# Kernel optimization log

Measured on AMD Instinct MI355X. Metric: run time of the kernel, lower is better.

The kernel has to match this reference:

```python
import jax, jax.numpy as jnp
import numpy as np

N, E, D = 50000, 800000, 128

def setup_inputs() -> dict:
    key = jax.random.key(0)
    ks = jax.random.split(key, 8)
    s = 0.02
    x = jax.random.normal(ks[0], (N, D), dtype=jnp.float32)
    edge_index = jax.random.randint(ks[1], (2, E), 0, N, dtype=jnp.int64)
    Wn = jax.random.normal(ks[2], (D, D), dtype=jnp.float32) * s
    bn = jax.random.normal(ks[3], (D,), dtype=jnp.float32) * s
    We = jax.random.normal(ks[4], (D, 2 * D), dtype=jnp.float32) * s
    be = jax.random.normal(ks[5], (D,), dtype=jnp.float32) * s
    Wu = jax.random.normal(ks[6], (D, 3 * D), dtype=jnp.float32) * s
    bu = jax.random.normal(ks[7], (D,), dtype=jnp.float32) * s
    return {"x": x, "edge_index": edge_index, "Wn": Wn, "bn": bn,
            "We": We, "be": be, "Wu": Wu, "bu": bu}

def reference(x, edge_index, Wn, bn, We, be, Wu, bu):
    n = x.shape[0]
    # 1. per-node linear transform (torch Linear: x @ W.T + b)
    node = x @ Wn.T + bn                                   # [N, D]
    src, dst = edge_index[0], edge_index[1]
    # 2. per-edge embedding from concatenated endpoint node embeddings
    edge_in = jnp.concatenate([node[src], node[dst]], axis=1)  # [E, 2D]
    edge_emb = edge_in @ We.T + be                          # [E, D]
    # 3. scatter-sum neighbor node embeddings and incident edge embeddings to src vertex
    nbr_sum = jax.ops.segment_sum(node[dst], src, num_segments=n)    # [N, D]
    edge_sum = jax.ops.segment_sum(edge_emb, src, num_segments=n)   # [N, D]
    pre_gelu = jnp.concatenate([node, nbr_sum, edge_sum], axis=1)    # [N, 3D]
    # 4-5. GELU (exact, matching torch nn.GELU default) + final linear
    out = jax.nn.gelu(pre_gelu, approximate=False) @ Wu.T + bu       # [N, D]
    return out
```

## Files before the change

kernel.cpp:

```cpp
#include <hip/hip_runtime.h>
#include <hip/hip_bf16.h>
#include <math.h>

typedef __attribute__((ext_vector_type(8))) short short8;
typedef __attribute__((ext_vector_type(4))) float f32x4;

#define CAP8 16
#define EPT  8

__device__ __forceinline__ float bf2f(unsigned short u) {
    union { unsigned int i; float f; } c; c.i = ((unsigned int)u) << 16; return c.f;
}
__device__ __forceinline__ unsigned short f2bf(float f) {
    __hip_bfloat16 h = __float2bfloat16(f);
    union { __hip_bfloat16 h; unsigned short u; } c; c.h = h; return c.u;
}
__device__ __forceinline__ float gelu_exact(float x) {
    return 0.5f * x * (1.0f + erff(x * 0.7071067811865475f));
}
__device__ __forceinline__ short8 ldcvt8(const float* p) {
    float4 f0 = *(const float4*)p;
    float4 f1 = *(const float4*)(p + 4);
    short8 a;
    a[0] = (short)f2bf(f0.x); a[1] = (short)f2bf(f0.y);
    a[2] = (short)f2bf(f0.z); a[3] = (short)f2bf(f0.w);
    a[4] = (short)f2bf(f1.x); a[5] = (short)f2bf(f1.y);
    a[6] = (short)f2bf(f1.z); a[7] = (short)f2bf(f1.w);
    return a;
}
__device__ __forceinline__ int swz(int row, int colbyte) {
    return row * 256 + (colbyte ^ ((row & 7) << 4));
}

__device__ __forceinline__ int detect_flag(const int* ei, int E) {
    int orv = 0;
    int lim = (E < 64) ? E : 64;
    for (int i = 0; i < lim; i++) orv |= ei[2 * i + 1];
    return (orv == 0) ? 1 : 0;
}
__device__ __forceinline__ int ld_src(const int* ei, int flag, int E, int e) {
    if (flag) { int2 p = *(const int2*)(ei + 2 * (size_t)e); return p.x; }
    return ei[e];
}
__device__ __forceinline__ int ld_dst(const int* ei, int flag, int E, int e) {
    if (flag) { int2 p = *(const int2*)(ei + 2 * (size_t)(E + e)); return p.x; }
    return ei[E + e];
}

__launch_bounds__(256)
__global__ void init_kernel(const float* __restrict__ Wn, const float* __restrict__ We,
                            const float* __restrict__ Wu,
                            unsigned short* __restrict__ Wnb, unsigned short* __restrict__ Web,
                            unsigned short* __restrict__ Wub,
                            int* __restrict__ cursor8, int N) {
    const int stride = gridDim.x * 256;
    const int t = blockIdx.x * 256 + threadIdx.x;
    for (int i = t; i < 8 * N; i += stride) cursor8[i] = 0;
    for (int i = t; i < 128 * 128; i += stride) Wnb[i] = f2bf(Wn[i]);
    for (int i = t; i < 128 * 256; i += stride) Web[i] = f2bf(We[i]);
    for (int i = t; i < 128 * 384; i += stride) Wub[i] = f2bf(Wu[i]);
}

__device__ __forceinline__ void gemm1_body(int bid,
                                           const float* __restrict__ x,
                                           const unsigned short* __restrict__ Wnb,
                                           const float* __restrict__ bias,
                                           unsigned short* __restrict__ node,
                                           unsigned short* __restrict__ Apre0,
                                           int N) {
    const int v0 = bid * 64;
    const int wave = threadIdx.x >> 6;
    const int lane = threadIdx.x & 63;
    const int m    = lane & 15;
    const int kq   = lane >> 4;

    short8 B[2][4];
#pragma unroll
    for (int ntl = 0; ntl < 2; ntl++) {
        const int j = (wave * 2 + ntl) * 16 + m;
#pragma unroll
        for (int kb = 0; kb < 4; kb++)
            B[ntl][kb] = *(const short8*)(Wnb + (size_t)j * 128 + kb * 32 + kq * 8);
    }

    f32x4 acc[4][2];
#pragma unroll
    for (int mt = 0; mt < 4; mt++)
#pragma unroll
        for (int ntl = 0; ntl < 2; ntl++) acc[mt][ntl] = (f32x4){0.f,0.f,0.f,0.f};

#pragma unroll
    for (int kb = 0; kb < 4; kb++) {
#pragma unroll
        for (int mt = 0; mt < 4; mt++) {
            const int row = v0 + mt * 16 + m;
            short8 a = (short8){0,0,0,0,0,0,0,0};
            if (row < N) a = ldcvt8(x + (size_t)row * 128 + kb * 32 + kq * 8);
#pragma unroll
            for (int ntl = 0; ntl < 2; ntl++)
                acc[mt][ntl] = __builtin_amdgcn_mfma_f32_16x16x32_bf16(a, B[ntl][kb], acc[mt][ntl], 0, 0, 0);
        }
    }

    const int ocol = lane & 15;
#pragma unroll
    for (int mt = 0; mt < 4; mt++) {
#pragma unroll
        for (int ntl = 0; ntl < 2; ntl++) {
            const int col = (wave * 2 + ntl) * 16 + ocol;
            const float bval = bias[col];
#pragma unroll
            for (int r = 0; r < 4; r++) {
                const int row = v0 + mt * 16 + (lane >> 4) * 4 + r;
                if (row < N) {
                    const float v = acc[mt][ntl][r] + bval;
                    node[(size_t)row * 128 + col]  = f2bf(v);
                    Apre0[(size_t)row * 128 + col] = f2bf(gelu_exact(v));
                }
            }
        }
    }
}

__launch_bounds__(256)
__global__ void fused_a(const float* __restrict__ x,
                        const unsigned short* __restrict__ Wnb,
                        const float* __restrict__ bn,
                        unsigned short* __restrict__ node,
                        unsigned short* __restrict__ Apre0,
                        const int* __restrict__ ei,
                        int* __restrict__ cursor8,
                        unsigned short* __restrict__ csr8,
                        int E, int N, int mblocks) {
    const int grp = blockIdx.x >> 3;
    if ((grp % 3) != 0) {
        const int g1 = grp - grp / 3 - 1;
        const int mid = g1 * 8 + (int)(blockIdx.x & 7);
        if (mid < mblocks) gemm1_body(mid, x, Wnb, bn, node, Apre0, N);
        return;
    }
    __shared__ int sflag;
    if (threadIdx.x == 0) sflag = detect_flag(ei, E);
    __syncthreads();
    const int fgrp = grp / 3;
    const int b = (int)(blockIdx.x & 7);
    const int e0 = (fgrp * 8 + b) * (256 * EPT) + (int)threadIdx.x;

    int sv[EPT], dv[EPT], p[EPT];
    bool ok[EPT];
#pragma unroll
    for (int k = 0; k < EPT; k++) {
        const int e = e0 + k * 256;
        ok[k] = (e < E);
        sv[k] = 0; dv[k] = 0; p[k] = CAP8;
        if (ok[k]) { sv[k] = ld_src(ei, sflag, E, e); dv[k] = ld_dst(ei, sflag, E, e); }
    }
#pragma unroll
    for (int k = 0; k < EPT; k++) {
        ok[k] = ok[k] && (unsigned)sv[k] < (unsigned)N && (unsigned)dv[k] < (unsigned)N;
        if (ok[k]) p[k] = atomicAdd(&cursor8[(size_t)b * N + sv[k]], 1);
    }
#pragma unroll
    for (int k = 0; k < EPT; k++) {
        if (ok[k] && p[k] < CAP8)
            csr8[((size_t)b * N + sv[k]) * CAP8 + p[k]] = (unsigned short)dv[k];
    }
}

#define G_ISSUE(I, B) { \
    const int vl_ = wave * 8 + (I); \
    dg_[B] = (v0 + vl_ < N) ? degI[vl_] : 0; \
    _Pragma("unroll") \
    for (int u = 0; u < 8; u++) { \
        const int r_ = way + u * 4; \
        const int id_ = (r_ < dg_[B]) ? (int)listT[vl_ * 128 + r_] : 0; \
        A_[B][u] = *(const short8*)(node + (size_t)id_ * 128 + sl * 8); \
    } }

#define G_CONSUME(I, B) { \
    const int vl_ = wave * 8 + (I); \
    const int v_  = v0 + vl_; \
    const int deg_ = dg_[B]; \
    float acc_[8] = {0.f,0.f,0.f,0.f,0.f,0.f,0.f,0.f}; \
    _Pragma("unroll") \
    for (int u = 0; u < 8; u++) { \
        const int r_ = way + u * 4; \
        if (r_ < deg_) { \
            _Pragma("unroll") \
            for (int k = 0; k < 8; k++) acc_[k] += bf2f((unsigned short)A_[B][u][k]); \
        } } \
    for (int base_ = 32; base_ < deg_; base_ += 32) {   \
        _Pragma("unroll") \
        for (int u = 0; u < 8; u++) { \
            const int r_ = base_ + way + u * 4; \
            const int id_ = (r_ < deg_) ? (int)listT[vl_ * 128 + r_] : 0; \
            short8 t_ = *(const short8*)(node + (size_t)id_ * 128 + sl * 8); \
            if (r_ < deg_) { \
                _Pragma("unroll") \
                for (int k = 0; k < 8; k++) acc_[k] += bf2f((unsigned short)t_[k]); \
            } } } \
    _Pragma("unroll") \
    for (int k = 0; k < 8; k++) { \
        acc_[k] += __shfl_xor(acc_[k], 16); \
        acc_[k] += __shfl_xor(acc_[k], 32); \
    } \
    if (v_ < N) { \
        if (way == 0) { \
            short8 o_; \
            _Pragma("unroll") \
            for (int k = 0; k < 8; k++) o_[k] = (short)f2bf(acc_[k]); \
            *(short8*)((char*)nbrT + swz(vl_, sl * 16)) = o_; \
        } else if (way == 1) { \
            short8 o_; \
            _Pragma("unroll") \
            for (int k = 0; k < 8; k++) o_[k] = (short)f2bf(gelu_exact(acc_[k])); \
            *(short8*)((char*)gnbrT + swz(vl_, sl * 16)) = o_; \
        } } }

__launch_bounds__(256)
__global__ void fused_b(const int* __restrict__ cursor8,
                        const unsigned short* __restrict__ csr8,
                        const unsigned short* __restrict__ node,
                        const unsigned short* __restrict__ Apre0,
                        const unsigned short* __restrict__ Web,
                        const float* __restrict__ be,
                        const unsigned short* __restrict__ Wub,
                        const float* __restrict__ bu,
                        float* __restrict__ out, int N) {
    __shared__ unsigned short nbrT [32 * 128];
    __shared__ unsigned short gnbrT[32 * 128];
    __shared__ unsigned short scratch[32 * 128];
    __shared__ int   degBv[32][8];
    __shared__ int   degI[32];
    __shared__ float degF[32];

    const int v0   = blockIdx.x * 32;
    const int tid  = threadIdx.x;
    const int wave = tid >> 6;
    const int lane = tid & 63;
    const int m    = lane & 15;
    const int kq   = lane >> 4;
    const bool full = (v0 + 32 <= N);

    {
        const int vi = tid >> 3, b = tid & 7;
        const int v = v0 + vi;
        int c = (v < N) ? cursor8[(size_t)b * N + v] : 0;
        degBv[vi][b] = (c > CAP8) ? CAP8 : c;
    }
    __syncthreads();
    if (tid < 32) {
        int s = 0;
#pragma unroll
        for (int b = 0; b < 8; b++) s += degBv[tid][b];
        degI[tid] = s; degF[tid] = (float)s;
    }
    __syncthreads();

    {
        unsigned short* listT = scratch;
#pragma unroll
        for (int i = 0; i < 8; i++) {
            const int vl = wave * 8 + i;
            const int v  = v0 + vl;
            if (v >= N) continue;
            const int slot0 = lane, slot1 = lane + 64;
            const unsigned short i0 = csr8[((size_t)(slot0 >> 4) * N + v) * CAP8 + (slot0 & 15)];
            const unsigned short i1 = csr8[((size_t)(slot1 >> 4) * N + v) * CAP8 + (slot1 & 15)];
            const bool vd0 = (slot0 & 15) < degBv[vl][slot0 >> 4];
            const bool vd1 = (slot1 & 15) < degBv[vl][slot1 >> 4];
            const unsigned long long m0 = __ballot(vd0);
            const unsigned long long m1 = __ballot(vd1);
            const unsigned long long below = (1ull << lane) - 1ull;
            const int n0 = __popcll(m0);
            if (vd0) listT[vl * 128 + __popcll(m0 & below)] = i0;
            if (vd1) listT[vl * 128 + n0 + __popcll(m1 & below)] = i1;
        }
        asm volatile("s_waitcnt lgkmcnt(0)" ::: "memory");

        const int way = lane >> 4, sl = lane & 15;
        short8 A_[2][8];
        int dg_[2];
        G_ISSUE(0, 0)
        G_ISSUE(1, 1)
        G_CONSUME(0, 0) G_ISSUE(2, 0)
        G_CONSUME(1, 1) G_ISSUE(3, 1)
        G_CONSUME(2, 0) G_ISSUE(4, 0)
        G_CONSUME(3, 1) G_ISSUE(5, 1)
        G_CONSUME(4, 0) G_ISSUE(6, 0)
        G_CONSUME(5, 1) G_ISSUE(7, 1)
        G_CONSUME(6, 0)
        G_CONSUME(7, 1)
    }
    __syncthreads();

    {
        f32x4 acc2[2][2];
#pragma unroll
        for (int mt = 0; mt < 2; mt++)
#pragma unroll
            for (int ntl = 0; ntl < 2; ntl++) acc2[mt][ntl] = (f32x4){0.f,0.f,0.f,0.f};

#pragma unroll
        for (int kb = 0; kb < 4; kb++) {
            short8 B0[2], B1[2], an[2], ab[2];
#pragma unroll
            for (int ntl = 0; ntl < 2; ntl++) {
                const int j = (wave * 2 + ntl) * 16 + m;
                B0[ntl] = *(const short8*)(Web + (size_t)j * 256 + kb * 32 + kq * 8);
                B1[ntl] = *(const short8*)(Web + (size_t)j * 256 + 128 + kb * 32 + kq * 8);
            }
#pragma unroll
            for (int mt = 0; mt < 2; mt++) {
                const int lrow = mt * 16 + m;
                const int row  = v0 + lrow;
                an[mt] = (full || row < N) ? *(const short8*)(node + (size_t)row * 128 + kb * 32 + kq * 8)
                                           : (short8){0,0,0,0,0,0,0,0};
                ab[mt] = *(const short8*)((const char*)nbrT + swz(lrow, kb * 64 + kq * 16));
            }
#pragma unroll
            for (int mt = 0; mt < 2; mt++) {
                const float dg = degF[mt * 16 + m];
#pragma unroll
                for (int k = 0; k < 8; k++)
                    an[mt][k] = (short)f2bf(dg * bf2f((unsigned short)an[mt][k]));
            }
#pragma unroll
            for (int mt = 0; mt < 2; mt++)
#pragma unroll
                for (int ntl = 0; ntl < 2; ntl++) {
                    acc2[mt][ntl] = __builtin_amdgcn_mfma_f32_16x16x32_bf16(an[mt], B0[ntl], acc2[mt][ntl], 0, 0, 0);
                    acc2[mt][ntl] = __builtin_amdgcn_mfma_f32_16x16x32_bf16(ab[mt], B1[ntl], acc2[mt][ntl], 0, 0, 0);
                }
        }

        const int ocol = lane & 15;
#pragma unroll
        for (int mt = 0; mt < 2; mt++) {
#pragma unroll
            for (int ntl = 0; ntl < 2; ntl++) {
                const int col = (wave * 2 + ntl) * 16 + ocol;
                const float bval = be[col];
#pragma unroll
                for (int r = 0; r < 4; r++) {
                    const int lrow = mt * 16 + (lane >> 4) * 4 + r;
                    const float dg = degF[lrow];
                    const float vv = gelu_exact(acc2[mt][ntl][r] + dg * bval);
                    *(unsigned short*)((char*)scratch + swz(lrow, col * 2)) = f2bf(vv);
                }
            }
        }
    }
    __syncthreads();

    {
        f32x4 acc3[2][2];
#pragma unroll
        for (int mt = 0; mt < 2; mt++)
#pragma unroll
            for (int ntl = 0; ntl < 2; ntl++) acc3[mt][ntl] = (f32x4){0.f,0.f,0.f,0.f};

#pragma unroll
        for (int s = 0; s < 3; s++) {
#pragma unroll
            for (int kb = 0; kb < 4; kb++) {
                short8 B3[2], a[2];
#pragma unroll
                for (int ntl = 0; ntl < 2; ntl++) {
                    const int j = (wave * 2 + ntl) * 16 + m;
                    B3[ntl] = *(const short8*)(Wub + (size_t)j * 384 + s * 128 + kb * 32 + kq * 8);
                }
#pragma unroll
                for (int mt = 0; mt < 2; mt++) {
                    const int lrow = mt * 16 + m;
                    const int row  = v0 + lrow;
                    if (s == 0) {
                        a[mt] = (full || row < N) ? *(const short8*)(Apre0 + (size_t)row * 128 + kb * 32 + kq * 8)
                                                  : (short8){0,0,0,0,0,0,0,0};
                    } else if (s == 1) {
                        a[mt] = *(const short8*)((const char*)gnbrT + swz(lrow, kb * 64 + kq * 16));
                    } else {
                        a[mt] = *(const short8*)((const char*)scratch + swz(lrow, kb * 64 + kq * 16));
                    }
                }
#pragma unroll
                for (int mt = 0; mt < 2; mt++)
#pragma unroll
                    for (int ntl = 0; ntl < 2; ntl++)
                        acc3[mt][ntl] = __builtin_amdgcn_mfma_f32_16x16x32_bf16(a[mt], B3[ntl], acc3[mt][ntl], 0, 0, 0);
            }
        }

        const int ocol = lane & 15;
#pragma unroll
        for (int mt = 0; mt < 2; mt++) {
#pragma unroll
            for (int ntl = 0; ntl < 2; ntl++) {
                const int col = (wave * 2 + ntl) * 16 + ocol;
                const float bval = bu[col];
#pragma unroll
                for (int r = 0; r < 4; r++) {
                    const int row = v0 + mt * 16 + (lane >> 4) * 4 + r;
                    if (row < N)
                        out[(size_t)row * 128 + col] = acc3[mt][ntl][r] + bval;
                }
            }
        }
    }
}

extern "C" void kernel_launch(void* const* d_in, const int* in_sizes, int n_in,
                              void* d_out, int out_size, void* d_ws, size_t ws_size,
                              hipStream_t stream) {
    const float* x  = (const float*)d_in[0];
    const int*   ei = (const int*)d_in[1];
    const float* Wn = (const float*)d_in[2];
    const float* bn = (const float*)d_in[3];
    const float* We = (const float*)d_in[4];
    const float* be = (const float*)d_in[5];
    const float* Wu = (const float*)d_in[6];
    const float* bu = (const float*)d_in[7];

    const int N = in_sizes[0] / 128;
    const int E = in_sizes[1] / 2;

    char* ws = (char*)d_ws;
    size_t off = 0;
    unsigned short* node  = (unsigned short*)(ws + off); off += (size_t)N * 128 * 2;
    unsigned short* Apre0 = (unsigned short*)(ws + off); off += (size_t)N * 128 * 2;
    off = (off + 255) & ~(size_t)255;
    int* cursor8 = (int*)(ws + off);                     off += (size_t)8 * N * 4;
    off = (off + 255) & ~(size_t)255;
    unsigned short* csr8 = (unsigned short*)(ws + off);  off += (size_t)8 * N * CAP8 * 2;
    off = (off + 255) & ~(size_t)255;
    unsigned short* Wnb = (unsigned short*)(ws + off);   off += (size_t)128 * 128 * 2;
    unsigned short* Web = (unsigned short*)(ws + off);   off += (size_t)128 * 256 * 2;
    unsigned short* Wub = (unsigned short*)(ws + off);   off += (size_t)128 * 384 * 2;

    const int mblocks = (N + 63) / 64;
    const int eblocks = (E + 256 * EPT - 1) / (256 * EPT);
    const int fgroups = (eblocks + 7) / 8;
    const int ggroups = (mblocks + 7) / 8;
    const int tgroups = fgroups + ggroups;
    const int grid_a  = tgroups * 8;

    init_kernel<<<512, 256, 0, stream>>>(Wn, We, Wu, Wnb, Web, Wub, cursor8, N);
    fused_a<<<grid_a, 256, 0, stream>>>(x, Wnb, bn, node, Apre0, ei, cursor8, csr8, E, N, mblocks);
    fused_b<<<(N + 31) / 32, 256, 0, stream>>>(cursor8, csr8, node, Apre0, Web, be, Wub, bu, (float*)d_out, N);
}
```

Baseline: 249.1 us.

## Stage neighbor gathers through LDS with async global_load_lds ring pipeline

Replaces the register double-buffered neighbor gather with direct global-to-LDS loads (global_load_lds) into a six-deep per-wave staging ring. Gathers are split into chunks of 8 neighbors and consumed after a vmcnt wait, with XOR swizzling on chunk columns to avoid bank conflicts. The goal is to keep more gather requests in flight without register pressure. The cost is 48KB of extra LDS, which may reduce occupancy, plus reliance on exact vmcnt accounting.

Measured after the change: 283.3 us. 13.7% more time.

```diff
diff --git a/kernel.cpp b/kernel.cpp
--- a/kernel.cpp
+++ b/kernel.cpp
@@ -30,6 +30,12 @@
 }
 __device__ __forceinline__ int swz(int row, int colbyte) {
     return row * 256 + (colbyte ^ ((row & 7) << 4));
+}
+
+typedef const __attribute__((address_space(1))) void* gas_p;
+typedef __attribute__((address_space(3))) void* las_p;
+__device__ __forceinline__ void gload_lds16(const void* g, void* l) {
+    __builtin_amdgcn_global_load_lds((gas_p)g, (las_p)l, 16, 0, 0);
 }
 
 __device__ __forceinline__ int detect_flag(const int* ei, int E) {
@@ -167,55 +173,67 @@
     }
 }
 
-#define G_ISSUE(I, B) { \
-    const int vl_ = wave * 8 + (I); \
-    dg_[B] = (v0 + vl_ < N) ? degI[vl_] : 0; \
+#define ISSUE(J) { \
+    constexpr int j_ = (J); \
+    if constexpr (j_ < 32) { \
+        const int vl_  = wv8 + (j_ >> 2); \
+        const int nb0_ = (j_ & 3) * 8; \
+        const int dgv_ = degI[vl_]; \
+        _Pragma("unroll") \
+        for (int i_ = 0; i_ < 2; i_++) { \
+            const int r_  = (lane >> 4) + 4 * i_;       \
+            const int n_  = nb0_ + r_; \
+            const int id_ = (n_ < dgv_) ? (int)listT[vl_ * 128 + n_] : 0; \
+            const int ch_ = (lane & 15) ^ r_;           \
+            gload_lds16(node + (size_t)id_ * 128 + ch_ * 8, &stag[wave][j_ % 6][4 * i_][0]); \
+        } } }
+
+#define CONS(J) { \
+    constexpr int j_ = (J); \
+    const int vl_  = wv8 + (j_ >> 2); \
+    const int nb0_ = (j_ & 3) * 8; \
+    const int dgv_ = degI[vl_]; \
+    asm volatile("s_waitcnt vmcnt(8)" ::: "memory"); \
+    __builtin_amdgcn_sched_barrier(0); \
     _Pragma("unroll") \
-    for (int u = 0; u < 8; u++) { \
-        const int r_ = way + u * 4; \
-        const int id_ = (r_ < dg_[B]) ? (int)listT[vl_ * 128 + r_] : 0; \
-        A_[B][u] = *(const short8*)(node + (size_t)id_ * 128 + sl * 8); \
-    } }
-
-#define G_CONSUME(I, B) { \
-    const int vl_ = wave * 8 + (I); \
-    const int v_  = v0 + vl_; \
-    const int deg_ = dg_[B]; \
-    float acc_[8] = {0.f,0.f,0.f,0.f,0.f,0.f,0.f,0.f}; \
-    _Pragma("unroll") \
-    for (int u = 0; u < 8; u++) { \
-        const int r_ = way + u * 4; \
-        if (r_ < deg_) { \
+    for (int i_ = 0; i_ < 2; i_++) { \
+        const int r_ = way + 4 * i_; \
+        if (nb0_ + r_ < dgv_) { \
+            short8 t_ = *(const short8*)&stag[wave][j_ % 6][r_][(sl ^ r_) * 8]; \
             _Pragma("unroll") \
-            for (int k = 0; k < 8; k++) acc_[k] += bf2f((unsigned short)A_[B][u][k]); \
+            for (int k = 0; k < 8; k++) acc[k] += bf2f((unsigned short)t_[k]); \
+        } } }
+
+#define FIN(V) { \
+    const int vl_  = wv8 + (V); \
+    const int v_   = v0 + vl_; \
+    const int dgv_ = degI[vl_]; \
+    if (__builtin_expect(dgv_ > 32, 0)) {               \
+        for (int n_ = 32 + way; n_ < dgv_; n_ += 4) { \
+            const int id_ = (int)listT[vl_ * 128 + n_]; \
+            short8 t_ = *(const short8*)(node + (size_t)id_ * 128 + sl * 8); \
+            _Pragma("unroll") \
+            for (int k = 0; k < 8; k++) acc[k] += bf2f((unsigned short)t_[k]); \
         } } \
-    for (int base_ = 32; base_ < deg_; base_ += 32) {   \
-        _Pragma("unroll") \
-        for (int u = 0; u < 8; u++) { \
-            const int r_ = base_ + way + u * 4; \
-            const int id_ = (r_ < deg_) ? (int)listT[vl_ * 128 + r_] : 0; \
-            short8 t_ = *(const short8*)(node + (size_t)id_ * 128 + sl * 8); \
-            if (r_ < deg_) { \
-                _Pragma("unroll") \
-                for (int k = 0; k < 8; k++) acc_[k] += bf2f((unsigned short)t_[k]); \
-            } } } \
     _Pragma("unroll") \
     for (int k = 0; k < 8; k++) { \
-        acc_[k] += __shfl_xor(acc_[k], 16); \
-        acc_[k] += __shfl_xor(acc_[k], 32); \
+        acc[k] += __shfl_xor(acc[k], 16); \
+        acc[k] += __shfl_xor(acc[k], 32); \
     } \
     if (v_ < N) { \
         if (way == 0) { \
             short8 o_; \
             _Pragma("unroll") \
-            for (int k = 0; k < 8; k++) o_[k] = (short)f2bf(acc_[k]); \
+            for (int k = 0; k < 8; k++) o_[k] = (short)f2bf(acc[k]); \
             *(short8*)((char*)nbrT + swz(vl_, sl * 16)) = o_; \
         } else if (way == 1) { \
             short8 o_; \
             _Pragma("unroll") \
-            for (int k = 0; k < 8; k++) o_[k] = (short)f2bf(gelu_exact(acc_[k])); \
+            for (int k = 0; k < 8; k++) o_[k] = (short)f2bf(gelu_exact(acc[k])); \
             *(short8*)((char*)gnbrT + swz(vl_, sl * 16)) = o_; \
-        } } }
+        } } \
+    _Pragma("unroll") \
+    for (int k = 0; k < 8; k++) acc[k] = 0.f; }
 
 __launch_bounds__(256)
 __global__ void fused_b(const int* __restrict__ cursor8,
@@ -230,6 +248,7 @@
     __shared__ unsigned short nbrT [32 * 128];
     __shared__ unsigned short gnbrT[32 * 128];
     __shared__ unsigned short scratch[32 * 128];
+    __shared__ unsigned short stag[4][6][8][128];
     __shared__ int   degBv[32][8];
     __shared__ int   degI[32];
     __shared__ float degF[32];
@@ -277,20 +296,45 @@
             if (vd1) listT[vl * 128 + n0 + __popcll(m1 & below)] = i1;
         }
         asm volatile("s_waitcnt lgkmcnt(0)" ::: "memory");
+        __builtin_amdgcn_sched_barrier(0);
 
         const int way = lane >> 4, sl = lane & 15;
-        short8 A_[2][8];
-        int dg_[2];
-        G_ISSUE(0, 0)
-        G_ISSUE(1, 1)
-        G_CONSUME(0, 0) G_ISSUE(2, 0)
-        G_CONSUME(1, 1) G_ISSUE(3, 1)
-        G_CONSUME(2, 0) G_ISSUE(4, 0)
-        G_CONSUME(3, 1) G_ISSUE(5, 1)
-        G_CONSUME(4, 0) G_ISSUE(6, 0)
-        G_CONSUME(5, 1) G_ISSUE(7, 1)
-        G_CONSUME(6, 0)
-        G_CONSUME(7, 1)
+        const int wv8 = wave * 8;
+        float acc[8] = {0.f,0.f,0.f,0.f,0.f,0.f,0.f,0.f};
+
+        ISSUE(0) ISSUE(1) ISSUE(2) ISSUE(3) ISSUE(4)
+        ISSUE(5)  CONS(0)
+        ISSUE(6)  CONS(1)
+        ISSUE(7)  CONS(2)
+        ISSUE(8)  CONS(3)  FIN(0)
+        ISSUE(9)  CONS(4)
+        ISSUE(10) CONS(5)
+        ISSUE(11) CONS(6)
+        ISSUE(12) CONS(7)  FIN(1)
+        ISSUE(13) CONS(8)
+        ISSUE(14) CONS(9)
+        ISSUE(15) CONS(10)
+        ISSUE(16) CONS(11) FIN(2)
+        ISSUE(17) CONS(12)
+        ISSUE(18) CONS(13)
+        ISSUE(19) CONS(14)
+        ISSUE(20) CONS(15) FIN(3)
+        ISSUE(21) CONS(16)
+        ISSUE(22) CONS(17)
+        ISSUE(23) CONS(18)
+        ISSUE(24) CONS(19) FIN(4)
+        ISSUE(25) CONS(20)
+        ISSUE(26) CONS(21)
+        ISSUE(27) CONS(22)
+        ISSUE(28) CONS(23) FIN(5)
+        ISSUE(29) CONS(24)
+        ISSUE(30) CONS(25)
+        ISSUE(31) CONS(26)
+        ISSUE(32) CONS(27) FIN(6)
+        ISSUE(33) CONS(28)
+        ISSUE(34) CONS(29)
+        ISSUE(35) CONS(30)
+        ISSUE(36) CONS(31) FIN(7)
     }
     __syncthreads();
 
```
